# Optimization experiments

Measured on AMD Instinct MI355X. Metric: run time of the kernel, lower is better.

The kernel has to match this reference:

```python
import jax, jax.numpy as jnp
import numpy as np

N = 100000        # nodes
E = 1_600_000     # edges (avg degree 16)
D_IN = 128        # input feature dim
H = 128           # hidden_channels


def _glorot(key, fan_in, fan_out):
    s = np.sqrt(1.0 / fan_in).astype(np.float32)
    return jax.random.uniform(key, (fan_in, fan_out), jnp.float32, -s, s)


def setup_inputs() -> dict:
    key = jax.random.key(0)
    ks = jax.random.split(key, 12)
    x = jax.random.normal(ks[0], (N, D_IN), jnp.float32)
    edge_index = jax.random.randint(ks[1], (2, E), 0, N, jnp.int32)
    edge_attr = jax.random.uniform(ks[2], (E,), jnp.float32)
    inp = {"x": x, "edge_index": edge_index, "edge_attr": edge_attr}
    dims = [(D_IN, H), (H, H), (H, H)]
    for i, (fi, fo) in enumerate(dims, start=1):
        inp[f"W_rel{i}"] = _glorot(ks[2 + 2 * i], fi, fo)
        inp[f"b{i}"] = jnp.zeros((fo,), jnp.float32)
        inp[f"W_root{i}"] = _glorot(ks[3 + 2 * i], fi, fo)
    return inp


def _graph_conv(x, src, dst, w, deg_inv, W_rel, b_rel, W_root):
    # message: x_j * edge_weight ; aggregate: mean over incoming edges
    msg = x[src] * w[:, None]                                   # [E, D]
    agg = jax.ops.segment_sum(msg, dst, num_segments=x.shape[0])
    agg = agg * deg_inv[:, None]                                # mean
    # GraphConv: lin_rel(agg) + lin_root(x); lin_rel has bias, lin_root none
    return agg @ W_rel + b_rel + x @ W_root


def reference(x, edge_index, edge_attr,
              W_rel1, b1, W_root1,
              W_rel2, b2, W_root2,
              W_rel3, b3, W_root3):
    src, dst = edge_index[0], edge_index[1]
    deg = jax.ops.segment_sum(jnp.ones((E,), x.dtype), dst, num_segments=N)
    deg_inv = jnp.where(deg > 0, 1.0 / deg, 0.0)
    h = jax.nn.relu(_graph_conv(x, src, dst, edge_attr, deg_inv, W_rel1, b1, W_root1))
    h = jax.nn.relu(_graph_conv(h, src, dst, edge_attr, deg_inv, W_rel2, b2, W_root2))
    # dropout(p=0.5) in eval mode -> identity
    h = jax.nn.relu(_graph_conv(h, src, dst, edge_attr, deg_inv, W_rel3, b3, W_root3))
    return h
```

## Files before the change

kernel.cpp:

```cpp
#include <hip/hip_runtime.h>
#include <hip/hip_bf16.h>


#define DIM 128
typedef unsigned short ushort_t;
typedef unsigned int uint_t;
typedef __attribute__((ext_vector_type(8))) short bf16x8;
typedef __attribute__((ext_vector_type(4))) float f32x4;

__device__ __forceinline__ ushort_t f2bf(float x) {
    uint_t u = __float_as_uint(x);
    u = (u + 0x7fff + ((u >> 16) & 1)) >> 16;
    return (ushort_t)u;
}
__device__ __forceinline__ float bf2f(ushort_t b) {
    return __uint_as_float(((uint_t)b) << 16);
}
__device__ __forceinline__ void gld_lds16(const void* g, void* s) {
    __builtin_amdgcn_global_load_lds((const __attribute__((address_space(1))) void*)g,
                                     (__attribute__((address_space(3))) void*)s, 16, 0, 0);
}

__global__ void hist_kernel(const int* __restrict__ dst, int* __restrict__ counts,
                            int* __restrict__ rank, int E) {
    int e = blockIdx.x * blockDim.x + threadIdx.x;
    if (e < E) rank[e] = atomicAdd(&counts[dst[e]], 1);
}

__global__ void assign_kernel(const int* __restrict__ counts, int* __restrict__ beg,
                              float* __restrict__ deg_inv, int* __restrict__ total, int n) {
    int i = blockIdx.x * blockDim.x + threadIdx.x;
    int lane = threadIdx.x & 63;
    int c = (i < n) ? counts[i] : 0;
    int s = c;
    #pragma unroll
    for (int off = 1; off < 64; off <<= 1) {
        int t = __shfl_up(s, off);
        if (lane >= off) s += t;
    }
    int wtot = __shfl(s, 63);
    int wbase = 0;
    if (lane == 63) wbase = atomicAdd(total, wtot);
    wbase = __shfl(wbase, 63);
    if (i < n) {
        beg[i] = wbase + s - c;
        deg_inv[i] = (c > 0) ? 1.0f / (float)c : 0.0f;
    }
}

__global__ void scatter_kernel(const int* __restrict__ edge_index,
                               const float* __restrict__ edge_attr,
                               const int* __restrict__ beg,
                               const int* __restrict__ rank,
                               int2* __restrict__ pk, int E) {
    int e = blockIdx.x * blockDim.x + threadIdx.x;
    if (e >= E) return;
    int s = edge_index[e];
    int d = edge_index[E + e];
    int pos = beg[d] + rank[e];
    int2 v; v.x = s; v.y = __float_as_int(edge_attr[e]);
    pk[pos] = v;
}

__global__ void split_kernel(const float* __restrict__ in, ushort_t* __restrict__ oh,
                             ushort_t* __restrict__ ol, int total4) {
    int i = blockIdx.x * blockDim.x + threadIdx.x;
    if (i >= total4) return;
    float4 v = *reinterpret_cast<const float4*>(&in[(size_t)i * 4]);
    ushort_t h0 = f2bf(v.x), h1 = f2bf(v.y), h2 = f2bf(v.z), h3 = f2bf(v.w);
    ushort_t l0 = f2bf(v.x - bf2f(h0)), l1 = f2bf(v.y - bf2f(h1));
    ushort_t l2 = f2bf(v.z - bf2f(h2)), l3 = f2bf(v.w - bf2f(h3));
    uint_t hw0 = (uint_t)h0 | ((uint_t)h1 << 16), hw1 = (uint_t)h2 | ((uint_t)h3 << 16);
    uint_t lw0 = (uint_t)l0 | ((uint_t)l1 << 16), lw1 = (uint_t)l2 | ((uint_t)l3 << 16);
    *reinterpret_cast<uint2*>(&oh[(size_t)i * 4]) = make_uint2(hw0, hw1);
    *reinterpret_cast<uint2*>(&ol[(size_t)i * 4]) = make_uint2(lw0, lw1);
}

__global__ void prep_w_kernel(const float* __restrict__ Wrel, const float* __restrict__ Wroot,
                              ushort_t* __restrict__ wh, ushort_t* __restrict__ wl) {
    int t = blockIdx.x * blockDim.x + threadIdx.x;
    if (t >= 32768) return;
    int q = t >> 3, j = t & 7;
    int kc = q >> 9, rem = q & 511, g = rem >> 7, nn = rem & 127;
    int k = kc * 32 + g * 8 + j;
    float v = (k < DIM) ? Wrel[k * DIM + nn] : Wroot[(k - DIM) * DIM + nn];
    ushort_t h = f2bf(v);
    wh[t] = h;
    wl[t] = f2bf(v - bf2f(h));
}

__global__ __launch_bounds__(256) void aggregate_kernel(
    const ushort_t* __restrict__ fh,
    const int2* __restrict__ pk,
    const int* __restrict__ beg, const int* __restrict__ counts,
    const float* __restrict__ deg_inv,
    ushort_t* __restrict__ ah, ushort_t* __restrict__ al, int n)
{
    int node = blockIdx.x * 4 + (threadIdx.x >> 6);
    if (node >= n) return;
    const int l = threadIdx.x & 63;
    int b   = __builtin_amdgcn_readfirstlane(beg[node]);
    int cnt = __builtin_amdgcn_readfirstlane(counts[node]);
    float a0 = 0.f, a1 = 0.f;
    int e = 0;
    for (; e + 8 <= cnt; e += 8) {
        int2 p[8];
        #pragma unroll
        for (int u = 0; u < 8; ++u) p[u] = pk[b + e + u];
        uint_t hb[8];
        #pragma unroll
        for (int u = 0; u < 8; ++u)
            hb[u] = *reinterpret_cast<const uint_t*>(&fh[(size_t)p[u].x * DIM + l * 2]);
        #pragma unroll
        for (int u = 0; u < 8; ++u) {
            float wt = __int_as_float(p[u].y);
            a0 = fmaf(bf2f((ushort_t)hb[u]), wt, a0);
            a1 = fmaf(bf2f((ushort_t)(hb[u] >> 16)), wt, a1);
        }
    }
    for (; e + 4 <= cnt; e += 4) {
        int2 p[4];
        #pragma unroll
        for (int u = 0; u < 4; ++u) p[u] = pk[b + e + u];
        #pragma unroll
        for (int u = 0; u < 4; ++u) {
            uint_t hb = *reinterpret_cast<const uint_t*>(&fh[(size_t)p[u].x * DIM + l * 2]);
            float wt = __int_as_float(p[u].y);
            a0 = fmaf(bf2f((ushort_t)hb), wt, a0);
            a1 = fmaf(bf2f((ushort_t)(hb >> 16)), wt, a1);
        }
    }
    for (; e < cnt; ++e) {
        int2 p = pk[b + e];
        uint_t hb = *reinterpret_cast<const uint_t*>(&fh[(size_t)p.x * DIM + l * 2]);
        float wt = __int_as_float(p.y);
        a0 = fmaf(bf2f((ushort_t)hb), wt, a0);
        a1 = fmaf(bf2f((ushort_t)(hb >> 16)), wt, a1);
    }
    float di = deg_inv[node];
    a0 *= di; a1 *= di;
    ushort_t h0 = f2bf(a0), h1 = f2bf(a1);
    uint_t hw = (uint_t)h0 | ((uint_t)h1 << 16);
    uint_t lw = (uint_t)f2bf(a0 - bf2f(h0)) | ((uint_t)f2bf(a1 - bf2f(h1)) << 16);
    size_t o = (size_t)node * DIM + l * 2;
    *reinterpret_cast<uint_t*>(&ah[o]) = hw;
    *reinterpret_cast<uint_t*>(&al[o]) = lw;
}

__global__ __launch_bounds__(256, 2) void gemm_mfma(
    const ushort_t* __restrict__ inh, const ushort_t* __restrict__ inl,
    const ushort_t* __restrict__ aggh, const ushort_t* __restrict__ aggl,
    const ushort_t* __restrict__ wh, const ushort_t* __restrict__ wl,
    const float* __restrict__ bias,
    float* __restrict__ outf, ushort_t* __restrict__ outh, ushort_t* __restrict__ outl,
    int n)
{
    __shared__ ushort_t lds[2][4][4096];
    const int tid = threadIdx.x;
    const int l = tid & 63;
    const int w = tid >> 6;
    const int m0 = blockIdx.x * 128;
    const int lr = l & 15, lg = l >> 4;
    const int rbase = (w >> 1) * 64, cbase = (w & 1) * 64;

    f32x4 acc[4][4];
    #pragma unroll
    for (int a = 0; a < 4; ++a)
        #pragma unroll
        for (int b = 0; b < 4; ++b) acc[a][b] = (f32x4){0.f, 0.f, 0.f, 0.f};

    auto stage = [&](int buf, int kc) {
        if (w < 2) {
            const ushort_t* src = (kc < 4) ? (w ? aggl : aggh) : (w ? inl : inh);
            const int kcl = (kc & 3) * 32;
            #pragma unroll
            for (int i = 0; i < 8; ++i) {
                int r = ((i & 1) << 6) + l;
                int g = i >> 1;
                gld_lds16(src + (size_t)(m0 + r) * DIM + kcl + g * 8,
                          &lds[buf][w][i << 9]);
            }
        } else {
            const ushort_t* src = ((w == 2) ? wh : wl) + (size_t)kc * 4096;
            #pragma unroll
            for (int i = 0; i < 8; ++i)
                gld_lds16(src + (size_t)(((i << 6) + l) * 8), &lds[buf][w][i << 9]);
        }
    };

    stage(0, 0);
    __syncthreads();
    int cur = 0;
    for (int kc = 0; kc < 8; ++kc) {
        if (kc < 7) stage(cur ^ 1, kc + 1);
        bf16x8 fah[4], fal[4], fwh[4], fwl[4];
        #pragma unroll
        for (int f = 0; f < 4; ++f) {
            int ar = rbase + f * 16 + lr;
            fah[f] = *reinterpret_cast<const bf16x8*>(&lds[cur][0][(lg * 128 + ar) * 8]);
            fal[f] = *reinterpret_cast<const bf16x8*>(&lds[cur][1][(lg * 128 + ar) * 8]);
            int cn = cbase + f * 16 + lr;
            fwh[f] = *reinterpret_cast<const bf16x8*>(&lds[cur][2][(lg * 128 + cn) * 8]);
            fwl[f] = *reinterpret_cast<const bf16x8*>(&lds[cur][3][(lg * 128 + cn) * 8]);
        }
        #pragma unroll
        for (int fm = 0; fm < 4; ++fm)
            #pragma unroll
            for (int fn = 0; fn < 4; ++fn) {
                acc[fm][fn] = __builtin_amdgcn_mfma_f32_16x16x32_bf16(fah[fm], fwh[fn], acc[fm][fn], 0, 0, 0);
                acc[fm][fn] = __builtin_amdgcn_mfma_f32_16x16x32_bf16(fah[fm], fwl[fn], acc[fm][fn], 0, 0, 0);
                acc[fm][fn] = __builtin_amdgcn_mfma_f32_16x16x32_bf16(fal[fm], fwh[fn], acc[fm][fn], 0, 0, 0);
            }
        __syncthreads();
        cur ^= 1;
    }

    #pragma unroll
    for (int fn = 0; fn < 4; ++fn) {
        int col = cbase + fn * 16 + lr;
        float bv = bias[col];
        #pragma unroll
        for (int fm = 0; fm < 4; ++fm) {
            int row0 = m0 + rbase + fm * 16 + lg * 4;
            #pragma unroll
            for (int e = 0; e < 4; ++e) {
                int row = row0 + e;
                if (row < n) {
                    float v = fmaxf(acc[fm][fn][e] + bv, 0.f);
                    size_t o = (size_t)row * DIM + col;
                    if (outf) outf[o] = v;
                    if (outh) {
                        ushort_t hb = f2bf(v);
                        outh[o] = hb;
                        outl[o] = f2bf(v - bf2f(hb));
                    }
                }
            }
        }
    }
}

extern "C" void kernel_launch(void* const* d_in, const int* in_sizes, int n_in,
                              void* d_out, int out_size, void* d_ws, size_t ws_size,
                              hipStream_t stream) {
    const float* x          = (const float*)d_in[0];
    const int*   edge_index = (const int*)d_in[1];
    const float* edge_attr  = (const float*)d_in[2];
    const float* Wrel1 = (const float*)d_in[3];
    const float* b1    = (const float*)d_in[4];
    const float* Wroot1= (const float*)d_in[5];
    const float* Wrel2 = (const float*)d_in[6];
    const float* b2    = (const float*)d_in[7];
    const float* Wroot2= (const float*)d_in[8];
    const float* Wrel3 = (const float*)d_in[9];
    const float* b3    = (const float*)d_in[10];
    const float* Wroot3= (const float*)d_in[11];

    const int N = in_sizes[0] / DIM;
    const int E = in_sizes[2];
    const size_t ND = (size_t)N * DIM;

    size_t off = 0;
    auto carve = [&](size_t bytes) -> char* {
        char* p = (char*)d_ws + off;
        off = (off + bytes + 255) & ~(size_t)255;
        return p;
    };
    int*   counts  = (int*)  carve((size_t)N * 4);
    int*   total   = (int*)  carve(256);
    size_t zero_end = off;
    int*   begb    = (int*)  carve((size_t)N * 4);
    float* deg_inv = (float*)carve((size_t)N * 4);
    int*   rank    = (int*)  carve((size_t)E * 4);
    int2*  pk      = (int2*) carve((size_t)E * 8);
    ushort_t* w1h = (ushort_t*)carve(65536);
    ushort_t* w1l = (ushort_t*)carve(65536);
    ushort_t* w2h = (ushort_t*)carve(65536);
    ushort_t* w2l = (ushort_t*)carve(65536);
    ushort_t* w3h = (ushort_t*)carve(65536);
    ushort_t* w3l = (ushort_t*)carve(65536);
    ushort_t* gh  = (ushort_t*)carve(ND * 2);
    ushort_t* gl  = (ushort_t*)carve(ND * 2);
    ushort_t* fxh = (ushort_t*)carve(ND * 2);
    ushort_t* fxl = (ushort_t*)carve(ND * 2);
    ushort_t* f1h = (ushort_t*)carve(ND * 2);
    ushort_t* f1l = (ushort_t*)carve(ND * 2);
    carve(32768);
    (void)ws_size; (void)n_in; (void)out_size;

    hipMemsetAsync(counts, 0, zero_end, stream);
    hist_kernel<<<(E + 255) / 256, 256, 0, stream>>>(edge_index + E, counts, rank, E);
    assign_kernel<<<(N + 255) / 256, 256, 0, stream>>>(counts, begb, deg_inv, total, N);
    scatter_kernel<<<(E + 255) / 256, 256, 0, stream>>>(edge_index, edge_attr, begb, rank, pk, E);

    split_kernel<<<(int)((ND / 4 + 255) / 256), 256, 0, stream>>>(x, fxh, fxl, (int)(ND / 4));
    prep_w_kernel<<<128, 256, 0, stream>>>(Wrel1, Wroot1, w1h, w1l);
    prep_w_kernel<<<128, 256, 0, stream>>>(Wrel2, Wroot2, w2h, w2l);
    prep_w_kernel<<<128, 256, 0, stream>>>(Wrel3, Wroot3, w3h, w3l);

    dim3 aggGrid((N + 3) / 4);
    dim3 gemmGrid((N + 127) / 128);

    aggregate_kernel<<<aggGrid, 256, 0, stream>>>(fxh, pk, begb, counts, deg_inv, gh, gl, N);
    gemm_mfma<<<gemmGrid, 256, 0, stream>>>(fxh, fxl, gh, gl, w1h, w1l, b1,
                                            nullptr, f1h, f1l, N);
    aggregate_kernel<<<aggGrid, 256, 0, stream>>>(f1h, pk, begb, counts, deg_inv, gh, gl, N);
    gemm_mfma<<<gemmGrid, 256, 0, stream>>>(f1h, f1l, gh, gl, w2h, w2l, b2,
                                            nullptr, fxh, fxl, N);
    aggregate_kernel<<<aggGrid, 256, 0, stream>>>(fxh, pk, begb, counts, deg_inv, gh, gl, N);
    gemm_mfma<<<gemmGrid, 256, 0, stream>>>(fxh, fxl, gh, gl, w3h, w3l, b3,
                                            (float*)d_out, nullptr, nullptr, N);
}
```

Measured before the change: 660.5 us.

## Replace split-bf16 three-pass GEMM with single fp16 MFMA and fp16 storage

Drops the hi/lo bf16 split representation for features, aggregates and weights and stores everything as single fp16. The GEMM now issues one f16 MFMA per tile instead of three bf16 MFMAs, stages half the LDS data, and raises the occupancy hint in launch_bounds. The low-part write and read traffic in convert, aggregate and GEMM epilogue is removed. In exchange, accuracy drops to fp16 precision with its narrower range, which risks tolerance failures.

After: 547.3 us. 1.21x faster.

```diff
diff --git a/kernel.cpp b/kernel.cpp
--- a/kernel.cpp
+++ b/kernel.cpp
@@ -1,20 +1,19 @@
 #include <hip/hip_runtime.h>
 #include <hip/hip_bf16.h>
+#include <hip/hip_fp16.h>
 
 
 #define DIM 128
 typedef unsigned short ushort_t;
 typedef unsigned int uint_t;
-typedef __attribute__((ext_vector_type(8))) short bf16x8;
+typedef __attribute__((ext_vector_type(8))) _Float16 f16x8;
 typedef __attribute__((ext_vector_type(4))) float f32x4;
 
-__device__ __forceinline__ ushort_t f2bf(float x) {
-    uint_t u = __float_as_uint(x);
-    u = (u + 0x7fff + ((u >> 16) & 1)) >> 16;
-    return (ushort_t)u;
-}
-__device__ __forceinline__ float bf2f(ushort_t b) {
-    return __uint_as_float(((uint_t)b) << 16);
+__device__ __forceinline__ ushort_t f2h(float x) {
+    return __half_as_ushort(__float2half(x));
+}
+__device__ __forceinline__ float h2f(ushort_t b) {
+    return __half2float(__ushort_as_half(b));
 }
 __device__ __forceinline__ void gld_lds16(const void* g, void* s) {
     __builtin_amdgcn_global_load_lds((const __attribute__((address_space(1))) void*)g,
@@ -62,31 +61,24 @@
     pk[pos] = v;
 }
 
-__global__ void split_kernel(const float* __restrict__ in, ushort_t* __restrict__ oh,
-                             ushort_t* __restrict__ ol, int total4) {
+__global__ void cvt_kernel(const float* __restrict__ in, ushort_t* __restrict__ oh, int total4) {
     int i = blockIdx.x * blockDim.x + threadIdx.x;
     if (i >= total4) return;
     float4 v = *reinterpret_cast<const float4*>(&in[(size_t)i * 4]);
-    ushort_t h0 = f2bf(v.x), h1 = f2bf(v.y), h2 = f2bf(v.z), h3 = f2bf(v.w);
-    ushort_t l0 = f2bf(v.x - bf2f(h0)), l1 = f2bf(v.y - bf2f(h1));
-    ushort_t l2 = f2bf(v.z - bf2f(h2)), l3 = f2bf(v.w - bf2f(h3));
-    uint_t hw0 = (uint_t)h0 | ((uint_t)h1 << 16), hw1 = (uint_t)h2 | ((uint_t)h3 << 16);
-    uint_t lw0 = (uint_t)l0 | ((uint_t)l1 << 16), lw1 = (uint_t)l2 | ((uint_t)l3 << 16);
-    *reinterpret_cast<uint2*>(&oh[(size_t)i * 4]) = make_uint2(hw0, hw1);
-    *reinterpret_cast<uint2*>(&ol[(size_t)i * 4]) = make_uint2(lw0, lw1);
+    ushort4 o;
+    o.x = f2h(v.x); o.y = f2h(v.y); o.z = f2h(v.z); o.w = f2h(v.w);
+    *reinterpret_cast<ushort4*>(&oh[(size_t)i * 4]) = o;
 }
 
 __global__ void prep_w_kernel(const float* __restrict__ Wrel, const float* __restrict__ Wroot,
-                              ushort_t* __restrict__ wh, ushort_t* __restrict__ wl) {
+                              ushort_t* __restrict__ wimg) {
     int t = blockIdx.x * blockDim.x + threadIdx.x;
     if (t >= 32768) return;
     int q = t >> 3, j = t & 7;
     int kc = q >> 9, rem = q & 511, g = rem >> 7, nn = rem & 127;
     int k = kc * 32 + g * 8 + j;
     float v = (k < DIM) ? Wrel[k * DIM + nn] : Wroot[(k - DIM) * DIM + nn];
-    ushort_t h = f2bf(v);
-    wh[t] = h;
-    wl[t] = f2bf(v - bf2f(h));
+    wimg[t] = f2h(v);
 }
 
 __global__ __launch_bounds__(256) void aggregate_kernel(
@@ -94,7 +86,7 @@
     const int2* __restrict__ pk,
     const int* __restrict__ beg, const int* __restrict__ counts,
     const float* __restrict__ deg_inv,
-    ushort_t* __restrict__ ah, ushort_t* __restrict__ al, int n)
+    ushort_t* __restrict__ ah, int n)
 {
     int node = blockIdx.x * 4 + (threadIdx.x >> 6);
     if (node >= n) return;
@@ -114,8 +106,8 @@
         #pragma unroll
         for (int u = 0; u < 8; ++u) {
             float wt = __int_as_float(p[u].y);
-            a0 = fmaf(bf2f((ushort_t)hb[u]), wt, a0);
-            a1 = fmaf(bf2f((ushort_t)(hb[u] >> 16)), wt, a1);
+            a0 = fmaf(h2f((ushort_t)hb[u]), wt, a0);
+            a1 = fmaf(h2f((ushort_t)(hb[u] >> 16)), wt, a1);
         }
     }
     for (; e + 4 <= cnt; e += 4) {
@@ -126,39 +118,36 @@
         for (int u = 0; u < 4; ++u) {
             uint_t hb = *reinterpret_cast<const uint_t*>(&fh[(size_t)p[u].x * DIM + l * 2]);
             float wt = __int_as_float(p[u].y);
-            a0 = fmaf(bf2f((ushort_t)hb), wt, a0);
-            a1 = fmaf(bf2f((ushort_t)(hb >> 16)), wt, a1);
+            a0 = fmaf(h2f((ushort_t)hb), wt, a0);
+            a1 = fmaf(h2f((ushort_t)(hb >> 16)), wt, a1);
         }
     }
     for (; e < cnt; ++e) {
         int2 p = pk[b + e];
         uint_t hb = *reinterpret_cast<const uint_t*>(&fh[(size_t)p.x * DIM + l * 2]);
         float wt = __int_as_float(p.y);
-        a0 = fmaf(bf2f((ushort_t)hb), wt, a0);
-        a1 = fmaf(bf2f((ushort_t)(hb >> 16)), wt, a1);
+        a0 = fmaf(h2f((ushort_t)hb), wt, a0);
+        a1 = fmaf(h2f((ushort_t)(hb >> 16)), wt, a1);
     }
     float di = deg_inv[node];
     a0 *= di; a1 *= di;
-    ushort_t h0 = f2bf(a0), h1 = f2bf(a1);
-    uint_t hw = (uint_t)h0 | ((uint_t)h1 << 16);
-    uint_t lw = (uint_t)f2bf(a0 - bf2f(h0)) | ((uint_t)f2bf(a1 - bf2f(h1)) << 16);
-    size_t o = (size_t)node * DIM + l * 2;
-    *reinterpret_cast<uint_t*>(&ah[o]) = hw;
-    *reinterpret_cast<uint_t*>(&al[o]) = lw;
-}
-
-__global__ __launch_bounds__(256, 2) void gemm_mfma(
-    const ushort_t* __restrict__ inh, const ushort_t* __restrict__ inl,
-    const ushort_t* __restrict__ aggh, const ushort_t* __restrict__ aggl,
-    const ushort_t* __restrict__ wh, const ushort_t* __restrict__ wl,
+    uint_t hw = (uint_t)f2h(a0) | ((uint_t)f2h(a1) << 16);
+    *reinterpret_cast<uint_t*>(&ah[(size_t)node * DIM + l * 2]) = hw;
+}
+
+__global__ __launch_bounds__(256, 4) void gemm_mfma(
+    const ushort_t* __restrict__ inh,
+    const ushort_t* __restrict__ aggh,
+    const ushort_t* __restrict__ wimg,
     const float* __restrict__ bias,
-    float* __restrict__ outf, ushort_t* __restrict__ outh, ushort_t* __restrict__ outl,
+    float* __restrict__ outf, ushort_t* __restrict__ outh,
     int n)
 {
-    __shared__ ushort_t lds[2][4][4096];
+    __shared__ ushort_t lds[2][2][4096];
     const int tid = threadIdx.x;
     const int l = tid & 63;
     const int w = tid >> 6;
+    const int ws = w & 1;
     const int m0 = blockIdx.x * 128;
     const int lr = l & 15, lg = l >> 4;
     const int rbase = (w >> 1) * 64, cbase = (w & 1) * 64;
@@ -171,20 +160,23 @@
 
     auto stage = [&](int buf, int kc) {
         if (w < 2) {
-            const ushort_t* src = (kc < 4) ? (w ? aggl : aggh) : (w ? inl : inh);
+            const ushort_t* src = (kc < 4) ? aggh : inh;
             const int kcl = (kc & 3) * 32;
             #pragma unroll
-            for (int i = 0; i < 8; ++i) {
-                int r = ((i & 1) << 6) + l;
-                int g = i >> 1;
+            for (int i = 0; i < 4; ++i) {
+                int q0 = ws * 256 + i * 64;
+                int q = q0 + l;
+                int g = q >> 7, r = q & 127;
                 gld_lds16(src + (size_t)(m0 + r) * DIM + kcl + g * 8,
-                          &lds[buf][w][i << 9]);
+                          &lds[buf][0][q0 * 8]);
             }
         } else {
-            const ushort_t* src = ((w == 2) ? wh : wl) + (size_t)kc * 4096;
-            #pragma unroll
-            for (int i = 0; i < 8; ++i)
-                gld_lds16(src + (size_t)(((i << 6) + l) * 8), &lds[buf][w][i << 9]);
+            const ushort_t* src = wimg + (size_t)kc * 4096;
+            #pragma unroll
+            for (int i = 0; i < 4; ++i) {
+                int q0 = ws * 256 + i * 64;
+                gld_lds16(src + (size_t)(q0 + l) * 8, &lds[buf][1][q0 * 8]);
+            }
         }
     };
 
@@ -193,24 +185,19 @@
     int cur = 0;
     for (int kc = 0; kc < 8; ++kc) {
         if (kc < 7) stage(cur ^ 1, kc + 1);
-        bf16x8 fah[4], fal[4], fwh[4], fwl[4];
+        f16x8 fa[4], fw[4];
         #pragma unroll
         for (int f = 0; f < 4; ++f) {
             int ar = rbase + f * 16 + lr;
-            fah[f] = *reinterpret_cast<const bf16x8*>(&lds[cur][0][(lg * 128 + ar) * 8]);
-            fal[f] = *reinterpret_cast<const bf16x8*>(&lds[cur][1][(lg * 128 + ar) * 8]);
+            fa[f] = *reinterpret_cast<const f16x8*>(&lds[cur][0][(lg * 128 + ar) * 8]);
             int cn = cbase + f * 16 + lr;
-            fwh[f] = *reinterpret_cast<const bf16x8*>(&lds[cur][2][(lg * 128 + cn) * 8]);
-            fwl[f] = *reinterpret_cast<const bf16x8*>(&lds[cur][3][(lg * 128 + cn) * 8]);
+            fw[f] = *reinterpret_cast<const f16x8*>(&lds[cur][1][(lg * 128 + cn) * 8]);
         }
         #pragma unroll
         for (int fm = 0; fm < 4; ++fm)
             #pragma unroll
-            for (int fn = 0; fn < 4; ++fn) {
-                acc[fm][fn] = __builtin_amdgcn_mfma_f32_16x16x32_bf16(fah[fm], fwh[fn], acc[fm][fn], 0, 0, 0);
-                acc[fm][fn] = __builtin_amdgcn_mfma_f32_16x16x32_bf16(fah[fm], fwl[fn], acc[fm][fn], 0, 0, 0);
-                acc[fm][fn] = __builtin_amdgcn_mfma_f32_16x16x32_bf16(fal[fm], fwh[fn], acc[fm][fn], 0, 0, 0);
-            }
+            for (int fn = 0; fn < 4; ++fn)
+                acc[fm][fn] = __builtin_amdgcn_mfma_f32_16x16x32_f16(fa[fm], fw[fn], acc[fm][fn], 0, 0, 0);
         __syncthreads();
         cur ^= 1;
     }
@@ -229,11 +216,7 @@
                     float v = fmaxf(acc[fm][fn][e] + bv, 0.f);
                     size_t o = (size_t)row * DIM + col;
                     if (outf) outf[o] = v;
-                    if (outh) {
-                        ushort_t hb = f2bf(v);
-                        outh[o] = hb;
-                        outl[o] = f2bf(v - bf2f(hb));
-                    }
+                    if (outh) outh[o] = f2h(v);
                 }
             }
         }
@@ -273,18 +256,12 @@
     float* deg_inv = (float*)carve((size_t)N * 4);
     int*   rank    = (int*)  carve((size_t)E * 4);
     int2*  pk      = (int2*) carve((size_t)E * 8);
-    ushort_t* w1h = (ushort_t*)carve(65536);
-    ushort_t* w1l = (ushort_t*)carve(65536);
-    ushort_t* w2h = (ushort_t*)carve(65536);
-    ushort_t* w2l = (ushort_t*)carve(65536);
-    ushort_t* w3h = (ushort_t*)carve(65536);
-    ushort_t* w3l = (ushort_t*)carve(65536);
-    ushort_t* gh  = (ushort_t*)carve(ND * 2);
-    ushort_t* gl  = (ushort_t*)carve(ND * 2);
-    ushort_t* fxh = (ushort_t*)carve(ND * 2);
-    ushort_t* fxl = (ushort_t*)carve(ND * 2);
-    ushort_t* f1h = (ushort_t*)carve(ND * 2);
-    ushort_t* f1l = (ushort_t*)carve(ND * 2);
+    ushort_t* w1 = (ushort_t*)carve(65536);
+    ushort_t* w2 = (ushort_t*)carve(65536);
+    ushort_t* w3 = (ushort_t*)carve(65536);
+    ushort_t* g  = (ushort_t*)carve(ND * 2);
+    ushort_t* fx = (ushort_t*)carve(ND * 2);
+    ushort_t* f1 = (ushort_t*)carve(ND * 2);
     carve(32768);
     (void)ws_size; (void)n_in; (void)out_size;
 
@@ -293,21 +270,18 @@
     assign_kernel<<<(N + 255) / 256, 256, 0, stream>>>(counts, begb, deg_inv, total, N);
     scatter_kernel<<<(E + 255) / 256, 256, 0, stream>>>(edge_index, edge_attr, begb, rank, pk, E);
 
-    split_kernel<<<(int)((ND / 4 + 255) / 256), 256, 0, stream>>>(x, fxh, fxl, (int)(ND / 4));
-    prep_w_kernel<<<128, 256, 0, stream>>>(Wrel1, Wroot1, w1h, w1l);
-    prep_w_kernel<<<128, 256, 0, stream>>>(Wrel2, Wroot2, w2h, w2l);
-    prep_w_kernel<<<128, 256, 0, stream>>>(Wrel3, Wroot3, w3h, w3l);
+    cvt_kernel<<<(int)((ND / 4 + 255) / 256), 256, 0, stream>>>(x, fx, (int)(ND / 4));
+    prep_w_kernel<<<128, 256, 0, stream>>>(Wrel1, Wroot1, w1);
+    prep_w_kernel<<<128, 256, 0, stream>>>(Wrel2, Wroot2, w2);
+    prep_w_kernel<<<128, 256, 0, stream>>>(Wrel3, Wroot3, w3);
 
     dim3 aggGrid((N + 3) / 4);
     dim3 gemmGrid((N + 127) / 128);
 
-    aggregate_kernel<<<aggGrid, 256, 0, stream>>>(fxh, pk, begb, counts, deg_inv, gh, gl, N);
-    gemm_mfma<<<gemmGrid, 256, 0, stream>>>(fxh, fxl, gh, gl, w1h, w1l, b1,
-                                            nullptr, f1h, f1l, N);
-    aggregate_kernel<<<aggGrid, 256, 0, stream>>>(f1h, pk, begb, counts, deg_inv, gh, gl, N);
-    gemm_mfma<<<gemmGrid, 256, 0, stream>>>(f1h, f1l, gh, gl, w2h, w2l, b2,
-                                            nullptr, fxh, fxl, N);
-    aggregate_kernel<<<aggGrid, 256, 0, stream>>>(fxh, pk, begb, counts, deg_inv, gh, gl, N);
-    gemm_mfma<<<gemmGrid, 256, 0, stream>>>(fxh, fxl, gh, gl, w3h, w3l, b3,
-                                            (float*)d_out, nullptr, nullptr, N);
-}
+    aggregate_kernel<<<aggGrid, 256, 0, stream>>>(fx, pk, begb, counts, deg_inv, g, N);
+    gemm_mfma<<<gemmGrid, 256, 0, stream>>>(fx, g, w1, b1, nullptr, f1, N);
+    aggregate_kernel<<<aggGrid, 256, 0, stream>>>(f1, pk, begb, counts, deg_inv, g, N);
+    gemm_mfma<<<gemmGrid, 256, 0, stream>>>(f1, g, w2, b2, nullptr, fx, N);
+    aggregate_kernel<<<aggGrid, 256, 0, stream>>>(fx, pk, begb, counts, deg_inv, g, N);
+    gemm_mfma<<<gemmGrid, 256, 0, stream>>>(fx, g, w3, b3, (float*)d_out, nullptr, N);
+}
```
